# Optimization experiments

Measured on AMD Instinct MI355X. Metric: run time of the kernel, lower is better.

## Reference

```python
import jax, jax.numpy as jnp
import numpy as np

EPS = 1e-5
N_CAMERAS, N_POINTS = 6, 4


def _bilinear_sample(feats, gx, gy):
    # feats: [B, C, H, W]; gx, gy: [B, Q] in [-1, 1]; align_corners=False, zero padding
    B, C, H, W = feats.shape
    ix = ((gx + 1.0) * W - 1.0) * 0.5
    iy = ((gy + 1.0) * H - 1.0) * 0.5
    x0 = jnp.floor(ix)
    y0 = jnp.floor(iy)
    fx = ix - x0
    fy = iy - y0
    x0i = x0.astype(jnp.int32)
    y0i = y0.astype(jnp.int32)
    ff = feats.reshape(B, C, H * W)

    def corner(xi, yi, w):
        valid = (xi >= 0) & (xi < W) & (yi >= 0) & (yi < H)
        idx = jnp.clip(yi, 0, H - 1) * W + jnp.clip(xi, 0, W - 1)
        v = jnp.take_along_axis(ff, idx[:, None, :], axis=2)  # [B, C, Q]
        return v * (w * valid)[:, None, :]

    return (corner(x0i, y0i, (1 - fx) * (1 - fy))
            + corner(x0i + 1, y0i, fx * (1 - fy))
            + corner(x0i, y0i + 1, (1 - fx) * fy)
            + corner(x0i + 1, y0i + 1, fx * fy))


def setup_inputs() -> dict:
    key = jax.random.key(0)
    ks = jax.random.split(key, 8)
    Hb = Wb = 128
    nq = Hb * Wb
    bs, hidden, N, P = 2, 256, N_CAMERAS, N_POINTS
    C, Hf, Wf = 256, 28, 50

    rho = jnp.broadcast_to((jnp.arange(Hb, dtype=jnp.float32) / Hb)[:, None], (Hb, Wb))
    phi = jnp.broadcast_to((jnp.arange(Wb, dtype=jnp.float32) / Wb)[None, :], (Hb, Wb))
    pc_range = jnp.array([51.2, 2.0 * np.pi, -5.0, 3.0], jnp.float32)
    intervals = jnp.array([51.2 / Hb, 2.0 * np.pi / Wb], jnp.float32)
    img_size = jnp.array([1600.0, 900.0], jnp.float32)

    # realistic pinhole lidar->image matrices for 6 surround cameras
    K = np.array([[1200.0, 0, 800, 0], [0, 1200.0, 450, 0], [0, 0, 1, 0], [0, 0, 0, 1]], np.float32)
    mats = []
    for i in range(N):
        yaw = 2.0 * np.pi * i / N
        c, s = np.cos(yaw), np.sin(yaw)
        R = np.array([[s, -c, 0], [0, 0, -1], [c, s, 0]], np.float32)  # x_right, y_down, z_forward
        E = np.eye(4, dtype=np.float32)
        E[:3, :3] = R
        E[:3, 3] = np.array([0.0, 1.5, 0.5], np.float32)
        mats.append(K @ E)
    lidar2imgs = jnp.asarray(np.broadcast_to(np.stack(mats), (bs, N, 4, 4)).copy())

    return {
        'query': jax.random.normal(ks[0], (nq, bs, hidden), jnp.float32),
        'query_pos': jax.random.normal(ks[1], (nq, bs, hidden), jnp.float32),
        'rho': rho,
        'phi': phi,
        'zz_cord': jax.random.uniform(ks[2], (bs, nq, 1), jnp.float32),
        'img_feats': jax.random.normal(ks[3], (bs, N, C, Hf, Wf), jnp.float32),
        'lidar2imgs': lidar2imgs,
        'intervals': intervals,
        'pc_range': pc_range,
        'img_size': img_size,
        'Wa': jax.random.normal(ks[4], (hidden, N * P), jnp.float32) * 0.02,
        'ba': jnp.zeros((N * P,), jnp.float32),
        'Wo': jax.random.normal(ks[5], (hidden, hidden), jnp.float32) * 0.02,
        'bo': jnp.zeros((hidden,), jnp.float32),
    }


def reference(query, query_pos, rho, phi, zz_cord, img_feats, lidar2imgs,
              intervals, pc_range, img_size, Wa, ba, Wo, bo):
    q = jnp.transpose(query + query_pos, (1, 0, 2))  # [bs, nq, h]
    bs, nq, _ = q.shape
    aw = (q @ Wa + ba).reshape(bs, 1, nq, N_CAMERAS, N_POINTS)

    # polar BEV -> cartesian lidar coords
    r = rho.reshape(-1, 1) * pc_range[0] + intervals[0] / 2  # [nq, 1]
    p = phi.reshape(-1, 1) * pc_range[1] - jnp.pi + intervals[1] / 2
    xx = r * jnp.cos(p)
    yy = r * jnp.sin(p)
    zz = zz_cord * (pc_range[3] - pc_range[2]) + pc_range[2]  # [bs, nq, 1]
    xyz = jnp.concatenate([
        jnp.broadcast_to(xx[None], (bs, nq, 1)),
        jnp.broadcast_to(yy[None], (bs, nq, 1)),
        zz,
        jnp.ones((bs, nq, 1), q.dtype),
    ], axis=-1)  # [bs, nq, 4]

    cam = jnp.einsum('bnij,bqj->bnqi', lidar2imgs, xyz)  # [bs, N, nq, 4]
    zc = cam[..., 2]
    gx = cam[..., 0] / jnp.maximum(zc, EPS) / img_size[0]
    gy = cam[..., 1] / jnp.maximum(zc, EPS) / img_size[1]
    gx = (gx - 0.5) * 2.0
    gy = (gy - 0.5) * 2.0
    mask = (zc > EPS) & (gx > -1.0) & (gx < 1.0) & (gy > -1.0) & (gy < 1.0)  # [bs, N, nq]

    B, N, C, H, W = img_feats.shape
    sampled = _bilinear_sample(img_feats.reshape(B * N, C, H, W),
                               gx.reshape(B * N, nq), gy.reshape(B * N, nq))
    sampled = jnp.nan_to_num(sampled.reshape(B, N, C, nq).transpose(0, 2, 3, 1))  # [bs, C, nq, N]

    maskf = mask.transpose(0, 2, 1)[:, None, :, :, None].astype(q.dtype)  # [bs,1,nq,N,1]
    ws = (jax.nn.sigmoid(aw) * maskf).sum(-1)  # [bs, 1, nq, N]
    out = jnp.einsum('bcqn,bqn->bcq', sampled, ws[:, 0])  # [bs, C, nq]
    out = out.transpose(2, 0, 1) @ Wo + bo + query  # dropout p=0 -> identity
    mask_out = mask.transpose(0, 2, 1)[:, None, :, :, None]  # [bs,1,nq,N,1] bool
    return out, mask_out
```

## Files before the change

kernel.cpp:

```cpp
#include <hip/hip_runtime.h>
#include <math.h>

#define NQ    16384
#define BS    2
#define HID   256
#define NCAM  6
#define NPTS  4
#define CF    256
#define HF    28
#define WF    50
#define HWF   (HF*WF)
#define NIMG  (BS*NCAM)
#define EPSV  1e-5f
#define GQ    16

typedef __attribute__((ext_vector_type(8))) short short8v;
typedef __attribute__((ext_vector_type(4))) float float4v;

__device__ __forceinline__ unsigned short f2bf(float f) {
    unsigned u = __float_as_uint(f);
    u += 0x7fffu + ((u >> 16) & 1u);
    return (unsigned short)(u >> 16);
}
__device__ __forceinline__ float bfLO(unsigned u) { return __uint_as_float(u << 16); }
__device__ __forceinline__ float bfHI(unsigned u) { return __uint_as_float(u & 0xffff0000u); }

__global__ __launch_bounds__(256) void transpose_feats(
    const float* __restrict__ feats, unsigned short* __restrict__ featsT)
{
    __shared__ float tile[32][33];
    const int img = blockIdx.x / 44;
    const int hw0 = (blockIdx.x % 44) * 32;
    const int tx = threadIdx.x & 31;
    const int ty = threadIdx.x >> 5;
    for (int ct = 0; ct < 8; ++ct) {
        const int c0 = ct * 32;
        #pragma unroll
        for (int i = 0; i < 4; ++i) {
            const int c  = c0 + ty + 8 * i;
            const int hw = hw0 + tx;
            tile[ty + 8 * i][tx] = (hw < HWF) ? feats[((size_t)img * CF + c) * HWF + hw] : 0.f;
        }
        __syncthreads();
        #pragma unroll
        for (int i = 0; i < 4; ++i) {
            const int hw = hw0 + ty + 8 * i;
            if (hw < HWF)
                featsT[((size_t)img * HWF + hw) * CF + c0 + tx] = f2bf(tile[tx][ty + 8 * i]);
        }
        __syncthreads();
    }
}

__global__ __launch_bounds__(256) void transpose_wo_wa(
    const float* __restrict__ Wo, const float* __restrict__ Wa,
    unsigned short* __restrict__ WoT, unsigned short* __restrict__ WaT)
{
    if (blockIdx.x < 64) {
        __shared__ float tile[32][33];
        const int kt = blockIdx.x >> 3, nt = blockIdx.x & 7;
        const int tx = threadIdx.x & 31;
        const int ty = threadIdx.x >> 5;
        #pragma unroll
        for (int i = 0; i < 4; ++i)
            tile[ty + 8 * i][tx] = Wo[(size_t)(kt * 32 + ty + 8 * i) * HID + nt * 32 + tx];
        __syncthreads();
        #pragma unroll
        for (int i = 0; i < 4; ++i)
            WoT[(size_t)(nt * 32 + ty + 8 * i) * HID + kt * 32 + tx] = f2bf(tile[tx][ty + 8 * i]);
    } else {
        #pragma unroll
        for (int v = 0; v < 4; ++v) {
            const int idx = (blockIdx.x - 64) * 1024 + v * 256 + threadIdx.x;
            const int j = idx >> 8, k = idx & 255;
            WaT[idx] = (j < 24) ? f2bf(Wa[k * 24 + j]) : (unsigned short)0;
        }
    }
}

__global__ __launch_bounds__(512) void ca_fused3(
    const float* __restrict__ query, const float* __restrict__ query_pos,
    const float* __restrict__ rho,   const float* __restrict__ phi,
    const float* __restrict__ zz,    const unsigned short* __restrict__ featsT,
    const float* __restrict__ l2i,   const float* __restrict__ intervals,
    const float* __restrict__ pc_range, const float* __restrict__ img_size,
    const unsigned short* __restrict__ WaT, const float* __restrict__ ba,
    const unsigned short* __restrict__ WoT, const float* __restrict__ bo,
    float* __restrict__ out)
{
    __shared__ char  fab[GQ * 512];
    __shared__ float awl[GQ][36];

    const int tid  = threadIdx.x;
    const int wave = tid >> 6;
    const int lane = tid & 63;
    const int l32  = lane & 31;
    const int r    = wave * 2 + (lane >> 5);
    const int base = blockIdx.x * GQ;
    const int g    = base + r;
    const int b    = g >> 14;
    const int q    = g & (NQ - 1);
    const size_t qrow = ((size_t)q * BS + b) * HID;

    {
        const float4 a0 = *reinterpret_cast<const float4*>(&query[qrow + 8 * l32]);
        const float4 a1 = *reinterpret_cast<const float4*>(&query[qrow + 8 * l32 + 4]);
        const float4 p0 = *reinterpret_cast<const float4*>(&query_pos[qrow + 8 * l32]);
        const float4 p1 = *reinterpret_cast<const float4*>(&query_pos[qrow + 8 * l32 + 4]);
        uint4 u;
        u.x = ((unsigned)f2bf(a0.y + p0.y) << 16) | f2bf(a0.x + p0.x);
        u.y = ((unsigned)f2bf(a0.w + p0.w) << 16) | f2bf(a0.z + p0.z);
        u.z = ((unsigned)f2bf(a1.y + p1.y) << 16) | f2bf(a1.x + p1.x);
        u.w = ((unsigned)f2bf(a1.w + p1.w) << 16) | f2bf(a1.z + p1.z);
        *reinterpret_cast<uint4*>(fab + ((unsigned)(r * 512 + 16 * l32) ^ ((unsigned)(r & 7) << 4))) = u;
    }

    float gxs[NCAM], gys[NCAM];
    bool  msk[NCAM];
    {
        const float pc0 = pc_range[0], pc1 = pc_range[1];
        const float pc2 = pc_range[2], pc3 = pc_range[3];
        const float rr = rho[q] * pc0 + intervals[0] * 0.5f;
        const float pp = phi[q] * pc1 - 3.14159265358979323846f + intervals[1] * 0.5f;
        const float xx = rr * cosf(pp);
        const float yy = rr * sinf(pp);
        const float z  = zz[b * NQ + q] * (pc3 - pc2) + pc2;
        const float iw = img_size[0], ih = img_size[1];
        #pragma unroll
        for (int n = 0; n < NCAM; ++n) {
            const float* M = l2i + (b * NCAM + n) * 16;
            const float cx = M[0]*xx + M[1]*yy + M[2]*z  + M[3];
            const float cy = M[4]*xx + M[5]*yy + M[6]*z  + M[7];
            const float cz = M[8]*xx + M[9]*yy + M[10]*z + M[11];
            const float d  = fmaxf(cz, EPSV);
            const float gx = (cx / d / iw - 0.5f) * 2.0f;
            const float gy = (cy / d / ih - 0.5f) * 2.0f;
            msk[n] = (cz > EPSV) && (gx > -1.0f) && (gx < 1.0f)
                                 && (gy > -1.0f) && (gy < 1.0f);
            gxs[n] = gx; gys[n] = gy;
        }
    }
    if (l32 < NCAM)
        out[(size_t)NQ * BS * HID + ((size_t)b * NQ + q) * NCAM + l32] =
            msk[l32] ? 1.0f : 0.0f;

    __syncthreads();

    if (wave < 2) {
        const int arow = lane & 15;
        const int g4   = lane >> 4;
        float4v aw = {0.f, 0.f, 0.f, 0.f};
        #pragma unroll
        for (int kk = 0; kk < 8; ++kk) {
            const int k0 = kk * 32 + g4 * 8;
            const short8v af = *reinterpret_cast<const short8v*>(
                fab + ((unsigned)(arow * 512 + k0 * 2) ^ ((unsigned)(arow & 7) << 4)));
            const short8v bw = *reinterpret_cast<const short8v*>(
                WaT + (size_t)(wave * 16 + arow) * HID + k0);
            aw = __builtin_amdgcn_mfma_f32_16x16x32_bf16(af, bw, aw, 0, 0, 0);
        }
        #pragma unroll
        for (int i = 0; i < 4; ++i)
            awl[g4 * 4 + i][wave * 16 + arow] = aw[i];
    }
    __syncthreads();

    float wsv[NCAM];
    {
        float sv = 0.f;
        if (l32 < 24) {
            const float x = awl[r][l32] + ba[l32];
            sv = 1.0f / (1.0f + __expf(-x));
        }
        sv += __shfl_xor(sv, 1);
        sv += __shfl_xor(sv, 2);
        #pragma unroll
        for (int n = 0; n < NCAM; ++n)
            wsv[n] = __shfl(sv, (lane & 32) + 4 * n);
    }

    float acc[8] = {0.f, 0.f, 0.f, 0.f, 0.f, 0.f, 0.f, 0.f};
    for (int n = 0; n < NCAM; ++n) {
        if (msk[n]) {
            const float ixf = ((gxs[n] + 1.0f) * WF - 1.0f) * 0.5f;
            const float iyf = ((gys[n] + 1.0f) * HF - 1.0f) * 0.5f;
            const float x0f = floorf(ixf), y0f = floorf(iyf);
            const float fx = ixf - x0f, fy = iyf - y0f;
            const int x0 = (int)x0f, y0 = (int)y0f;
            const int   xs[4] = {x0, x0 + 1, x0,     x0 + 1};
            const int   ys[4] = {y0, y0,     y0 + 1, y0 + 1};
            const float wc[4] = {(1.f-fx)*(1.f-fy), fx*(1.f-fy),
                                 (1.f-fx)*fy,       fx*fy};
            const unsigned short* fb = featsT + (size_t)(b * NCAM + n) * HWF * CF + 8 * l32;
            #pragma unroll
            for (int c4 = 0; c4 < 4; ++c4) {
                const bool v = (xs[c4] >= 0) && (xs[c4] < WF) &&
                               (ys[c4] >= 0) && (ys[c4] < HF);
                const int xc = min(max(xs[c4], 0), WF - 1);
                const int yc = min(max(ys[c4], 0), HF - 1);
                const float wnv = wsv[n] * (v ? wc[c4] : 0.0f);
                const uint4 u = *reinterpret_cast<const uint4*>(fb + (size_t)(yc * WF + xc) * CF);
                acc[0] += wnv * bfLO(u.x); acc[1] += wnv * bfHI(u.x);
                acc[2] += wnv * bfLO(u.y); acc[3] += wnv * bfHI(u.y);
                acc[4] += wnv * bfLO(u.z); acc[5] += wnv * bfHI(u.z);
                acc[6] += wnv * bfLO(u.w); acc[7] += wnv * bfHI(u.w);
            }
        }
    }

    {
        uint4 u;
        u.x = ((unsigned)f2bf(acc[1]) << 16) | f2bf(acc[0]);
        u.y = ((unsigned)f2bf(acc[3]) << 16) | f2bf(acc[2]);
        u.z = ((unsigned)f2bf(acc[5]) << 16) | f2bf(acc[4]);
        u.w = ((unsigned)f2bf(acc[7]) << 16) | f2bf(acc[6]);
        *reinterpret_cast<uint4*>(fab + ((unsigned)(r * 512 + 16 * l32) ^ ((unsigned)(r & 7) << 4))) = u;
    }
    __syncthreads();

    const int colw = lane & 15;
    const int g4   = lane >> 4;
    #pragma unroll
    for (int t = 0; t < 2; ++t) {
        const int col = wave * 16 + t * 128 + colw;
        float4v dacc = {0.f, 0.f, 0.f, 0.f};
        #pragma unroll
        for (int kk = 0; kk < 8; ++kk) {
            const int k0 = kk * 32 + g4 * 8;
            const short8v af = *reinterpret_cast<const short8v*>(
                fab + ((unsigned)(colw * 512 + k0 * 2) ^ ((unsigned)(colw & 7) << 4)));
            const short8v bw = *reinterpret_cast<const short8v*>(
                WoT + (size_t)col * HID + k0);
            dacc = __builtin_amdgcn_mfma_f32_16x16x32_bf16(af, bw, dacc, 0, 0, 0);
        }
        #pragma unroll
        for (int rg = 0; rg < 4; ++rg) {
            const int rowq = g4 * 4 + rg;
            const int gq = base + rowq;
            const int bq = gq >> 14, qq = gq & (NQ - 1);
            const size_t addr = ((size_t)qq * BS + bq) * HID + col;
            out[addr] = dacc[rg] + bo[col] + query[addr];
        }
    }
}

#define CHUNK 32
__global__ __launch_bounds__(512, 2) void ca_fused_fb(
    const float* __restrict__ query, const float* __restrict__ query_pos,
    const float* __restrict__ rho, const float* __restrict__ phi,
    const float* __restrict__ zz, const float* __restrict__ feats,
    const float* __restrict__ l2i, const float* __restrict__ intervals,
    const float* __restrict__ pc_range, const float* __restrict__ img_size,
    const float* __restrict__ Wa, const float* __restrict__ ba,
    const float* __restrict__ Wo, const float* __restrict__ bo,
    float* __restrict__ out)
{
    __shared__ float fa[8][HID];
    __shared__ float wolds[CHUNK][HID];
    const int tid  = threadIdx.x;
    const int wave = tid >> 6;
    const int lane = tid & 63;
    const int g    = blockIdx.x * 8 + wave;
    const int b    = g / NQ;
    const int q    = g - b * NQ;
    const size_t qrow = ((size_t)q * BS + b) * HID;
    {
        float qv[4];
        #pragma unroll
        for (int k = 0; k < 4; ++k) {
            const int h = lane + 64 * k;
            qv[k] = query[qrow + h] + query_pos[qrow + h];
        }
        const float pc0 = pc_range[0], pc1 = pc_range[1];
        const float pc2 = pc_range[2], pc3 = pc_range[3];
        const float r = rho[q] * pc0 + intervals[0] * 0.5f;
        const float p = phi[q] * pc1 - 3.14159265358979323846f + intervals[1] * 0.5f;
        const float xx = r * cosf(p);
        const float yy = r * sinf(p);
        const float z  = zz[b * NQ + q] * (pc3 - pc2) + pc2;
        const float iw = img_size[0], ih = img_size[1];
        float gxs[NCAM], gys[NCAM], wss[NCAM];
        bool  msk[NCAM];
        #pragma unroll
        for (int n = 0; n < NCAM; ++n) {
            const float* M = l2i + (b * NCAM + n) * 16;
            const float cx = M[0]*xx + M[1]*yy + M[2]*z  + M[3];
            const float cy = M[4]*xx + M[5]*yy + M[6]*z  + M[7];
            const float cz = M[8]*xx + M[9]*yy + M[10]*z + M[11];
            const float d  = fmaxf(cz, EPSV);
            const float gx = (cx / d / iw - 0.5f) * 2.0f;
            const float gy = (cy / d / ih - 0.5f) * 2.0f;
            msk[n] = (cz > EPSV) && (gx > -1.0f) && (gx < 1.0f)
                                 && (gy > -1.0f) && (gy < 1.0f);
            gxs[n] = gx; gys[n] = gy; wss[n] = 0.0f;
        }
        for (int n = 0; n < NCAM; ++n) {
            if (!msk[n]) continue;
            float s = 0.0f;
            #pragma unroll
            for (int pp = 0; pp < NPTS; ++pp) {
                const int j = n * NPTS + pp;
                float part = 0.0f;
                #pragma unroll
                for (int k = 0; k < 4; ++k)
                    part += qv[k] * Wa[(lane + 64 * k) * 24 + j];
                #pragma unroll
                for (int off = 32; off; off >>= 1)
                    part += __shfl_xor(part, off, 64);
                s += 1.0f / (1.0f + expf(-(part + ba[j])));
            }
            wss[n] = s;
        }
        if (lane < NCAM)
            out[(size_t)NQ * BS * HID + ((size_t)b * NQ + q) * NCAM + lane] =
                msk[lane] ? 1.0f : 0.0f;
        float acc[4] = {0.f, 0.f, 0.f, 0.f};
        for (int n = 0; n < NCAM; ++n) {
            if (!msk[n]) continue;
            const float ixf = ((gxs[n] + 1.0f) * WF - 1.0f) * 0.5f;
            const float iyf = ((gys[n] + 1.0f) * HF - 1.0f) * 0.5f;
            const float x0f = floorf(ixf), y0f = floorf(iyf);
            const float fx = ixf - x0f, fy = iyf - y0f;
            const int x0 = (int)x0f, y0 = (int)y0f;
            const int   xs[4] = {x0, x0 + 1, x0,     x0 + 1};
            const int   ys[4] = {y0, y0,     y0 + 1, y0 + 1};
            const float wc[4] = {(1.f-fx)*(1.f-fy), fx*(1.f-fy),
                                 (1.f-fx)*fy,       fx*fy};
            int   offc[4];
            float wv[4];
            #pragma unroll
            for (int c4 = 0; c4 < 4; ++c4) {
                const bool v = (xs[c4] >= 0) && (xs[c4] < WF) &&
                               (ys[c4] >= 0) && (ys[c4] < HF);
                const int xc = min(max(xs[c4], 0), WF - 1);
                const int yc = min(max(ys[c4], 0), HF - 1);
                offc[c4] = yc * WF + xc;
                wv[c4]   = v ? wc[c4] : 0.0f;
            }
            const float wn = wss[n];
            const float* fbp = feats + (size_t)(b * NCAM + n) * CF * HWF;
            #pragma unroll
            for (int k = 0; k < 4; ++k) {
                const float* fc = fbp + (size_t)(lane + 64 * k) * HWF;
                const float sv = wv[0]*fc[offc[0]] + wv[1]*fc[offc[1]]
                               + wv[2]*fc[offc[2]] + wv[3]*fc[offc[3]];
                acc[k] += wn * sv;
            }
        }
        #pragma unroll
        for (int k = 0; k < 4; ++k)
            fa[wave][lane + 64 * k] = acc[k];
    }
    float racc[4] = {0.f, 0.f, 0.f, 0.f};
    const int h0 = 4 * lane;
    for (int c0 = 0; c0 < HID; c0 += CHUNK) {
        __syncthreads();
        for (int i = tid; i < CHUNK * HID; i += 512)
            wolds[i >> 8][i & 255] = Wo[(size_t)(c0 + (i >> 8)) * HID + (i & 255)];
        __syncthreads();
        #pragma unroll 8
        for (int c = 0; c < CHUNK; ++c) {
            const float fav = fa[wave][c0 + c];
            const float4 wv4 = *reinterpret_cast<const float4*>(&wolds[c][h0]);
            racc[0] += fav * wv4.x;
            racc[1] += fav * wv4.y;
            racc[2] += fav * wv4.z;
            racc[3] += fav * wv4.w;
        }
    }
    float4 o;
    o.x = racc[0] + bo[h0 + 0] + query[qrow + h0 + 0];
    o.y = racc[1] + bo[h0 + 1] + query[qrow + h0 + 1];
    o.z = racc[2] + bo[h0 + 2] + query[qrow + h0 + 2];
    o.w = racc[3] + bo[h0 + 3] + query[qrow + h0 + 3];
    *reinterpret_cast<float4*>(&out[qrow + h0]) = o;
}

extern "C" void kernel_launch(void* const* d_in, const int* in_sizes, int n_in,
                              void* d_out, int out_size, void* d_ws, size_t ws_size,
                              hipStream_t stream) {
    const float* query     = (const float*)d_in[0];
    const float* query_pos = (const float*)d_in[1];
    const float* rho       = (const float*)d_in[2];
    const float* phi       = (const float*)d_in[3];
    const float* zz        = (const float*)d_in[4];
    const float* feats     = (const float*)d_in[5];
    const float* l2i       = (const float*)d_in[6];
    const float* intervals = (const float*)d_in[7];
    const float* pc_range  = (const float*)d_in[8];
    const float* img_size  = (const float*)d_in[9];
    const float* Wa        = (const float*)d_in[10];
    const float* ba        = (const float*)d_in[11];
    const float* Wo        = (const float*)d_in[12];
    const float* bo        = (const float*)d_in[13];
    float* out = (float*)d_out;

    const size_t featsT_bytes = (size_t)NIMG * HWF * CF * 2;
    const size_t woT_bytes    = (size_t)HID * HID * 2;
    const size_t waT_bytes    = (size_t)32 * HID * 2;
    const size_t need = featsT_bytes + woT_bytes + waT_bytes;

    if (ws_size >= need) {
        unsigned short* featsT = (unsigned short*)d_ws;
        unsigned short* WoT    = (unsigned short*)((char*)d_ws + featsT_bytes);
        unsigned short* WaT    = (unsigned short*)((char*)d_ws + featsT_bytes + woT_bytes);
        transpose_feats<<<NIMG * 44, 256, 0, stream>>>(feats, featsT);
        transpose_wo_wa<<<72, 256, 0, stream>>>(Wo, Wa, WoT, WaT);
        ca_fused3<<<(BS * NQ) / GQ, 512, 0, stream>>>(query, query_pos, rho, phi, zz,
                                                      featsT, l2i, intervals, pc_range,
                                                      img_size, WaT, ba, WoT, bo, out);
    } else {
        ca_fused_fb<<<(BS * NQ) / 8, 512, 0, stream>>>(query, query_pos, rho, phi, zz,
                                                       feats, l2i, intervals, pc_range,
                                                       img_size, Wa, ba, Wo, bo, out);
    }
}
```

Baseline: 79.48 us.

## Split fused kernel into attention-weight, gather and tiled GEMM kernels

```diff
diff --git a/kernel.cpp b/kernel.cpp
--- a/kernel.cpp
+++ b/kernel.cpp
@@ -12,7 +12,6 @@
 #define HWF   (HF*WF)
 #define NIMG  (BS*NCAM)
 #define EPSV  1e-5f
-#define GQ    16
 
 typedef __attribute__((ext_vector_type(8))) short short8v;
 typedef __attribute__((ext_vector_type(4))) float float4v;
@@ -25,42 +24,37 @@
 __device__ __forceinline__ float bfLO(unsigned u) { return __uint_as_float(u << 16); }
 __device__ __forceinline__ float bfHI(unsigned u) { return __uint_as_float(u & 0xffff0000u); }
 
-__global__ __launch_bounds__(256) void transpose_feats(
-    const float* __restrict__ feats, unsigned short* __restrict__ featsT)
+__global__ __launch_bounds__(256) void prep_all(
+    const float* __restrict__ feats, const float* __restrict__ Wo,
+    const float* __restrict__ Wa, unsigned short* __restrict__ featsT,
+    unsigned short* __restrict__ WoT, unsigned short* __restrict__ WaT)
 {
     __shared__ float tile[32][33];
-    const int img = blockIdx.x / 44;
-    const int hw0 = (blockIdx.x % 44) * 32;
     const int tx = threadIdx.x & 31;
     const int ty = threadIdx.x >> 5;
-    for (int ct = 0; ct < 8; ++ct) {
-        const int c0 = ct * 32;
-        #pragma unroll
-        for (int i = 0; i < 4; ++i) {
-            const int c  = c0 + ty + 8 * i;
-            const int hw = hw0 + tx;
-            tile[ty + 8 * i][tx] = (hw < HWF) ? feats[((size_t)img * CF + c) * HWF + hw] : 0.f;
-        }
-        __syncthreads();
-        #pragma unroll
-        for (int i = 0; i < 4; ++i) {
-            const int hw = hw0 + ty + 8 * i;
-            if (hw < HWF)
-                featsT[((size_t)img * HWF + hw) * CF + c0 + tx] = f2bf(tile[tx][ty + 8 * i]);
-        }
-        __syncthreads();
-    }
-}
-
-__global__ __launch_bounds__(256) void transpose_wo_wa(
-    const float* __restrict__ Wo, const float* __restrict__ Wa,
-    unsigned short* __restrict__ WoT, unsigned short* __restrict__ WaT)
-{
-    if (blockIdx.x < 64) {
-        __shared__ float tile[32][33];
-        const int kt = blockIdx.x >> 3, nt = blockIdx.x & 7;
-        const int tx = threadIdx.x & 31;
-        const int ty = threadIdx.x >> 5;
+    if (blockIdx.x < 528) {
+        const int img = blockIdx.x / 44;
+        const int hw0 = (blockIdx.x % 44) * 32;
+        for (int ct = 0; ct < 8; ++ct) {
+            const int c0 = ct * 32;
+            #pragma unroll
+            for (int i = 0; i < 4; ++i) {
+                const int c  = c0 + ty + 8 * i;
+                const int hw = hw0 + tx;
+                tile[ty + 8 * i][tx] = (hw < HWF) ? feats[((size_t)img * CF + c) * HWF + hw] : 0.f;
+            }
+            __syncthreads();
+            #pragma unroll
+            for (int i = 0; i < 4; ++i) {
+                const int hw = hw0 + ty + 8 * i;
+                if (hw < HWF)
+                    featsT[((size_t)img * HWF + hw) * CF + c0 + tx] = f2bf(tile[tx][ty + 8 * i]);
+            }
+            __syncthreads();
+        }
+    } else if (blockIdx.x < 592) {
+        const int bid = blockIdx.x - 528;
+        const int kt = bid >> 3, nt = bid & 7;
         #pragma unroll
         for (int i = 0; i < 4; ++i)
             tile[ty + 8 * i][tx] = Wo[(size_t)(kt * 32 + ty + 8 * i) * HID + nt * 32 + tx];
@@ -69,54 +63,85 @@
         for (int i = 0; i < 4; ++i)
             WoT[(size_t)(nt * 32 + ty + 8 * i) * HID + kt * 32 + tx] = f2bf(tile[tx][ty + 8 * i]);
     } else {
+        const int bid = blockIdx.x - 592;
         #pragma unroll
         for (int v = 0; v < 4; ++v) {
-            const int idx = (blockIdx.x - 64) * 1024 + v * 256 + threadIdx.x;
+            const int idx = bid * 1024 + v * 256 + threadIdx.x;
             const int j = idx >> 8, k = idx & 255;
             WaT[idx] = (j < 24) ? f2bf(Wa[k * 24 + j]) : (unsigned short)0;
         }
     }
 }
 
-__global__ __launch_bounds__(512) void ca_fused3(
+__global__ __launch_bounds__(256) void k_aw(
     const float* __restrict__ query, const float* __restrict__ query_pos,
-    const float* __restrict__ rho,   const float* __restrict__ phi,
-    const float* __restrict__ zz,    const unsigned short* __restrict__ featsT,
-    const float* __restrict__ l2i,   const float* __restrict__ intervals,
+    const unsigned short* __restrict__ WaT, const float* __restrict__ ba,
+    float* __restrict__ ws)
+{
+    const int wave = threadIdx.x >> 6;
+    const int lane = threadIdx.x & 63;
+    const int arow = lane & 15;
+    const int g4   = lane >> 4;
+    const int g0   = (blockIdx.x * 4 + wave) * 16;
+    const int ga   = g0 + arow;
+    const int bb   = ga >> 14;
+    const int qq   = ga & (NQ - 1);
+    const float* qp1 = query     + ((size_t)qq * BS + bb) * HID;
+    const float* qp2 = query_pos + ((size_t)qq * BS + bb) * HID;
+
+    float4v aw0 = {0.f,0.f,0.f,0.f}, aw1 = {0.f,0.f,0.f,0.f};
+    #pragma unroll
+    for (int kk = 0; kk < 8; ++kk) {
+        const int k0 = kk * 32 + g4 * 8;
+        const float4 a0 = *reinterpret_cast<const float4*>(qp1 + k0);
+        const float4 a1 = *reinterpret_cast<const float4*>(qp1 + k0 + 4);
+        const float4 p0 = *reinterpret_cast<const float4*>(qp2 + k0);
+        const float4 p1 = *reinterpret_cast<const float4*>(qp2 + k0 + 4);
+        short8v af;
+        af[0] = (short)f2bf(a0.x + p0.x); af[1] = (short)f2bf(a0.y + p0.y);
+        af[2] = (short)f2bf(a0.z + p0.z); af[3] = (short)f2bf(a0.w + p0.w);
+        af[4] = (short)f2bf(a1.x + p1.x); af[5] = (short)f2bf(a1.y + p1.y);
+        af[6] = (short)f2bf(a1.z + p1.z); af[7] = (short)f2bf(a1.w + p1.w);
+        const short8v b0 = *reinterpret_cast<const short8v*>(WaT + (size_t)arow * HID + k0);
+        const short8v b1 = *reinterpret_cast<const short8v*>(WaT + (size_t)(16 + arow) * HID + k0);
+        aw0 = __builtin_amdgcn_mfma_f32_16x16x32_bf16(af, b0, aw0, 0, 0, 0);
+        aw1 = __builtin_amdgcn_mfma_f32_16x16x32_bf16(af, b1, aw1, 0, 0, 0);
+    }
+    const float ba0 = ba[arow];
+    const float ba1 = (arow < 8) ? ba[16 + arow] : 0.f;
+    #pragma unroll
+    for (int i = 0; i < 4; ++i) {
+        float s0 = 1.0f / (1.0f + __expf(-(aw0[i] + ba0)));
+        float s1 = (arow < 8) ? 1.0f / (1.0f + __expf(-(aw1[i] + ba1))) : 0.f;
+        s0 += __shfl_xor(s0, 1);  s0 += __shfl_xor(s0, 2);
+        s1 += __shfl_xor(s1, 1);  s1 += __shfl_xor(s1, 2);
+        if ((arow & 3) == 0) {
+            const int gq = g0 + g4 * 4 + i;
+            ws[(size_t)gq * 8 + (arow >> 2)] = s0;
+            if (arow < 8)
+                ws[(size_t)gq * 8 + 4 + (arow >> 2)] = s1;
+        }
+    }
+}
+
+__global__ __launch_bounds__(512) void k_gather(
+    const float* __restrict__ rho, const float* __restrict__ phi,
+    const float* __restrict__ zz, const unsigned short* __restrict__ featsT,
+    const float* __restrict__ l2i, const float* __restrict__ intervals,
     const float* __restrict__ pc_range, const float* __restrict__ img_size,
-    const unsigned short* __restrict__ WaT, const float* __restrict__ ba,
-    const unsigned short* __restrict__ WoT, const float* __restrict__ bo,
+    const float* __restrict__ ws, unsigned short* __restrict__ fa,
     float* __restrict__ out)
 {
-    __shared__ char  fab[GQ * 512];
-    __shared__ float awl[GQ][36];
-
-    const int tid  = threadIdx.x;
-    const int wave = tid >> 6;
-    const int lane = tid & 63;
+    const int lane = threadIdx.x & 63;
+    const int wave = threadIdx.x >> 6;
     const int l32  = lane & 31;
     const int r    = wave * 2 + (lane >> 5);
-    const int base = blockIdx.x * GQ;
-    const int g    = base + r;
+    const int g    = blockIdx.x * 16 + r;
     const int b    = g >> 14;
     const int q    = g & (NQ - 1);
-    const size_t qrow = ((size_t)q * BS + b) * HID;
-
-    {
-        const float4 a0 = *reinterpret_cast<const float4*>(&query[qrow + 8 * l32]);
-        const float4 a1 = *reinterpret_cast<const float4*>(&query[qrow + 8 * l32 + 4]);
-        const float4 p0 = *reinterpret_cast<const float4*>(&query_pos[qrow + 8 * l32]);
-        const float4 p1 = *reinterpret_cast<const float4*>(&query_pos[qrow + 8 * l32 + 4]);
-        uint4 u;
-        u.x = ((unsigned)f2bf(a0.y + p0.y) << 16) | f2bf(a0.x + p0.x);
-        u.y = ((unsigned)f2bf(a0.w + p0.w) << 16) | f2bf(a0.z + p0.z);
-        u.z = ((unsigned)f2bf(a1.y + p1.y) << 16) | f2bf(a1.x + p1.x);
-        u.w = ((unsigned)f2bf(a1.w + p1.w) << 16) | f2bf(a1.z + p1.z);
-        *reinterpret_cast<uint4*>(fab + ((unsigned)(r * 512 + 16 * l32) ^ ((unsigned)(r & 7) << 4))) = u;
-    }
-
+
+    bool  msk[NCAM];
     float gxs[NCAM], gys[NCAM];
-    bool  msk[NCAM];
     {
         const float pc0 = pc_range[0], pc1 = pc_range[1];
         const float pc2 = pc_range[2], pc3 = pc_range[3];
@@ -140,16 +165,196 @@
             gxs[n] = gx; gys[n] = gy;
         }
     }
+    {
+        unsigned mbits = 0;
+        #pragma unroll
+        for (int n = 0; n < NCAM; ++n) mbits |= (msk[n] ? 1u : 0u) << n;
+        if (l32 < NCAM)
+            out[(size_t)NQ * BS * HID + ((size_t)b * NQ + q) * NCAM + l32] =
+                ((mbits >> l32) & 1u) ? 1.0f : 0.0f;
+    }
+
+    float wsv[NCAM];
+    {
+        const float wsn = ws[(size_t)g * 8 + (l32 & 7)];
+        #pragma unroll
+        for (int n = 0; n < NCAM; ++n)
+            wsv[n] = msk[n] ? __shfl(wsn, (lane & 32) + n) : 0.f;
+    }
+
+    float acc[8] = {0.f,0.f,0.f,0.f,0.f,0.f,0.f,0.f};
+    for (int n = 0; n < NCAM; ++n) {
+        if (!msk[n]) continue;
+        const float ixf = ((gxs[n] + 1.0f) * WF - 1.0f) * 0.5f;
+        const float iyf = ((gys[n] + 1.0f) * HF - 1.0f) * 0.5f;
+        const float x0f = floorf(ixf), y0f = floorf(iyf);
+        const float fx = ixf - x0f, fy = iyf - y0f;
+        const int x0 = (int)x0f, y0 = (int)y0f;
+        const int   xs[4] = {x0, x0 + 1, x0,     x0 + 1};
+        const int   ys[4] = {y0, y0,     y0 + 1, y0 + 1};
+        const float wc[4] = {(1.f-fx)*(1.f-fy), fx*(1.f-fy),
+                             (1.f-fx)*fy,       fx*fy};
+        const unsigned short* fb = featsT + (size_t)(b * NCAM + n) * HWF * CF + 8 * l32;
+        #pragma unroll
+        for (int c4 = 0; c4 < 4; ++c4) {
+            const bool v = (xs[c4] >= 0) && (xs[c4] < WF) &&
+                           (ys[c4] >= 0) && (ys[c4] < HF);
+            const int xc = min(max(xs[c4], 0), WF - 1);
+            const int yc = min(max(ys[c4], 0), HF - 1);
+            const float w = wsv[n] * (v ? wc[c4] : 0.0f);
+            const uint4 u = *reinterpret_cast<const uint4*>(fb + (size_t)(yc * WF + xc) * CF);
+            acc[0] += w * bfLO(u.x); acc[1] += w * bfHI(u.x);
+            acc[2] += w * bfLO(u.y); acc[3] += w * bfHI(u.y);
+            acc[4] += w * bfLO(u.z); acc[5] += w * bfHI(u.z);
+            acc[6] += w * bfLO(u.w); acc[7] += w * bfHI(u.w);
+        }
+    }
+
+    uint4 u;
+    u.x = ((unsigned)f2bf(acc[1]) << 16) | f2bf(acc[0]);
+    u.y = ((unsigned)f2bf(acc[3]) << 16) | f2bf(acc[2]);
+    u.z = ((unsigned)f2bf(acc[5]) << 16) | f2bf(acc[4]);
+    u.w = ((unsigned)f2bf(acc[7]) << 16) | f2bf(acc[6]);
+    *reinterpret_cast<uint4*>(fa + (size_t)g * HID + 8 * l32) = u;
+}
+
+__global__ __launch_bounds__(512) void k_gemm(
+    const unsigned short* __restrict__ fa, const unsigned short* __restrict__ WoT,
+    const float* __restrict__ bo, const float* __restrict__ query,
+    float* __restrict__ out)
+{
+    const int wave = threadIdx.x >> 6;
+    const int lane = threadIdx.x & 63;
+    const int arow = lane & 15;
+    const int g4   = lane >> 4;
+    const int wm   = wave >> 2;
+    const int wn   = wave & 3;
+    const int m0   = blockIdx.x * 128;
+
+    const unsigned short* aptr = fa  + (size_t)(m0 + wm * 64 + arow) * HID;
+    const unsigned short* bptr = WoT + (size_t)(wn * 64 + arow) * HID;
+
+    float4v acc00={0.f,0.f,0.f,0.f}, acc01={0.f,0.f,0.f,0.f}, acc02={0.f,0.f,0.f,0.f}, acc03={0.f,0.f,0.f,0.f};
+    float4v acc10={0.f,0.f,0.f,0.f}, acc11={0.f,0.f,0.f,0.f}, acc12={0.f,0.f,0.f,0.f}, acc13={0.f,0.f,0.f,0.f};
+    float4v acc20={0.f,0.f,0.f,0.f}, acc21={0.f,0.f,0.f,0.f}, acc22={0.f,0.f,0.f,0.f}, acc23={0.f,0.f,0.f,0.f};
+    float4v acc30={0.f,0.f,0.f,0.f}, acc31={0.f,0.f,0.f,0.f}, acc32={0.f,0.f,0.f,0.f}, acc33={0.f,0.f,0.f,0.f};
+
+    #pragma unroll 2
+    for (int kk = 0; kk < 8; ++kk) {
+        const int k0 = kk * 32 + g4 * 8;
+        short8v af0 = *reinterpret_cast<const short8v*>(aptr + 0 * 16 * HID + k0);
+        short8v af1 = *reinterpret_cast<const short8v*>(aptr + 1 * 16 * HID + k0);
+        short8v af2 = *reinterpret_cast<const short8v*>(aptr + 2 * 16 * HID + k0);
+        short8v af3 = *reinterpret_cast<const short8v*>(aptr + 3 * 16 * HID + k0);
+        short8v bf0 = *reinterpret_cast<const short8v*>(bptr + 0 * 16 * HID + k0);
+        short8v bf1 = *reinterpret_cast<const short8v*>(bptr + 1 * 16 * HID + k0);
+        short8v bf2 = *reinterpret_cast<const short8v*>(bptr + 2 * 16 * HID + k0);
+        short8v bf3 = *reinterpret_cast<const short8v*>(bptr + 3 * 16 * HID + k0);
+        acc00 = __builtin_amdgcn_mfma_f32_16x16x32_bf16(af0, bf0, acc00, 0, 0, 0);
+        acc01 = __builtin_amdgcn_mfma_f32_16x16x32_bf16(af0, bf1, acc01, 0, 0, 0);
+        acc02 = __builtin_amdgcn_mfma_f32_16x16x32_bf16(af0, bf2, acc02, 0, 0, 0);
+        acc03 = __builtin_amdgcn_mfma_f32_16x16x32_bf16(af0, bf3, acc03, 0, 0, 0);
+        acc10 = __builtin_amdgcn_mfma_f32_16x16x32_bf16(af1, bf0, acc10, 0, 0, 0);
+        acc11 = __builtin_amdgcn_mfma_f32_16x16x32_bf16(af1, bf1, acc11, 0, 0, 0);
+        acc12 = __builtin_amdgcn_mfma_f32_16x16x32_bf16(af1, bf2, acc12, 0, 0, 0);
+        acc13 = __builtin_amdgcn_mfma_f32_16x16x32_bf16(af1, bf3, acc13, 0, 0, 0);
+        acc20 = __builtin_amdgcn_mfma_f32_16x16x32_bf16(af2, bf0, acc20, 0, 0, 0);
+        acc21 = __builtin_amdgcn_mfma_f32_16x16x32_bf16(af2, bf1, acc21, 0, 0, 0);
+        acc22 = __builtin_amdgcn_mfma_f32_16x16x32_bf16(af2, bf2, acc22, 0, 0, 0);
+        acc23 = __builtin_amdgcn_mfma_f32_16x16x32_bf16(af2, bf3, acc23, 0, 0, 0);
+        acc30 = __builtin_amdgcn_mfma_f32_16x16x32_bf16(af3, bf0, acc30, 0, 0, 0);
+        acc31 = __builtin_amdgcn_mfma_f32_16x16x32_bf16(af3, bf1, acc31, 0, 0, 0);
+        acc32 = __builtin_amdgcn_mfma_f32_16x16x32_bf16(af3, bf2, acc32, 0, 0, 0);
+        acc33 = __builtin_amdgcn_mfma_f32_16x16x32_bf16(af3, bf3, acc33, 0, 0, 0);
+    }
+
+    float4v* accs[4][4] = {{&acc00,&acc01,&acc02,&acc03},{&acc10,&acc11,&acc12,&acc13},
+                           {&acc20,&acc21,&acc22,&acc23},{&acc30,&acc31,&acc32,&acc33}};
+    #pragma unroll
+    for (int j = 0; j < 4; ++j) {
+        const int col = wn * 64 + j * 16 + arow;
+        const float boc = bo[col];
+        #pragma unroll
+        for (int i = 0; i < 4; ++i) {
+            const float4v av = *accs[i][j];
+            #pragma unroll
+            for (int rg = 0; rg < 4; ++rg) {
+                const int m  = m0 + wm * 64 + i * 16 + g4 * 4 + rg;
+                const int bq = m >> 14, qq = m & (NQ - 1);
+                const size_t addr = ((size_t)qq * BS + bq) * HID + col;
+                out[addr] = av[rg] + boc + query[addr];
+            }
+        }
+    }
+}
+
+__global__ __launch_bounds__(512) void ca_fused3(
+    const float* __restrict__ query, const float* __restrict__ query_pos,
+    const float* __restrict__ rho,   const float* __restrict__ phi,
+    const float* __restrict__ zz,    const unsigned short* __restrict__ featsT,
+    const float* __restrict__ l2i,   const float* __restrict__ intervals,
+    const float* __restrict__ pc_range, const float* __restrict__ img_size,
+    const unsigned short* __restrict__ WaT, const float* __restrict__ ba,
+    const unsigned short* __restrict__ WoT, const float* __restrict__ bo,
+    float* __restrict__ out)
+{
+    __shared__ char  fab[16 * 512];
+    __shared__ float awl[16][36];
+    const int tid  = threadIdx.x;
+    const int wave = tid >> 6;
+    const int lane = tid & 63;
+    const int l32  = lane & 31;
+    const int r    = wave * 2 + (lane >> 5);
+    const int base = blockIdx.x * 16;
+    const int g    = base + r;
+    const int b    = g >> 14;
+    const int q    = g & (NQ - 1);
+    const size_t qrow = ((size_t)q * BS + b) * HID;
+    {
+        const float4 a0 = *reinterpret_cast<const float4*>(&query[qrow + 8 * l32]);
+        const float4 a1 = *reinterpret_cast<const float4*>(&query[qrow + 8 * l32 + 4]);
+        const float4 p0 = *reinterpret_cast<const float4*>(&query_pos[qrow + 8 * l32]);
+        const float4 p1 = *reinterpret_cast<const float4*>(&query_pos[qrow + 8 * l32 + 4]);
+        uint4 u;
+        u.x = ((unsigned)f2bf(a0.y + p0.y) << 16) | f2bf(a0.x + p0.x);
+        u.y = ((unsigned)f2bf(a0.w + p0.w) << 16) | f2bf(a0.z + p0.z);
+        u.z = ((unsigned)f2bf(a1.y + p1.y) << 16) | f2bf(a1.x + p1.x);
+        u.w = ((unsigned)f2bf(a1.w + p1.w) << 16) | f2bf(a1.z + p1.z);
+        *reinterpret_cast<uint4*>(fab + ((unsigned)(r * 512 + 16 * l32) ^ ((unsigned)(r & 7) << 4))) = u;
+    }
+    float gxs[NCAM], gys[NCAM];
+    bool  msk[NCAM];
+    {
+        const float pc0 = pc_range[0], pc1 = pc_range[1];
+        const float pc2 = pc_range[2], pc3 = pc_range[3];
+        const float rr = rho[q] * pc0 + intervals[0] * 0.5f;
+        const float pp = phi[q] * pc1 - 3.14159265358979323846f + intervals[1] * 0.5f;
+        const float xx = rr * cosf(pp);
+        const float yy = rr * sinf(pp);
+        const float z  = zz[b * NQ + q] * (pc3 - pc2) + pc2;
+        const float iw = img_size[0], ih = img_size[1];
+        #pragma unroll
+        for (int n = 0; n < NCAM; ++n) {
+            const float* M = l2i + (b * NCAM + n) * 16;
+            const float cx = M[0]*xx + M[1]*yy + M[2]*z  + M[3];
+            const float cy = M[4]*xx + M[5]*yy + M[6]*z  + M[7];
+            const float cz = M[8]*xx + M[9]*yy + M[10]*z + M[11];
+            const float d  = fmaxf(cz, EPSV);
+            const float gx = (cx / d / iw - 0.5f) * 2.0f;
+            const float gy = (cy / d / ih - 0.5f) * 2.0f;
+            msk[n] = (cz > EPSV) && (gx > -1.0f) && (gx < 1.0f)
+                                 && (gy > -1.0f) && (gy < 1.0f);
+            gxs[n] = gx; gys[n] = gy;
+        }
+    }
     if (l32 < NCAM)
         out[(size_t)NQ * BS * HID + ((size_t)b * NQ + q) * NCAM + l32] =
             msk[l32] ? 1.0f : 0.0f;
-
     __syncthreads();
-
     if (wave < 2) {
         const int arow = lane & 15;
         const int g4   = lane >> 4;
-        float4v aw = {0.f, 0.f, 0.f, 0.f};
+        float4v aw = {0.f,0.f,0.f,0.f};
         #pragma unroll
         for (int kk = 0; kk < 8; ++kk) {
             const int k0 = kk * 32 + g4 * 8;
@@ -164,7 +369,6 @@
             awl[g4 * 4 + i][wave * 16 + arow] = aw[i];
     }
     __syncthreads();
-
     float wsv[NCAM];
     {
         float sv = 0.f;
@@ -178,8 +382,7 @@
         for (int n = 0; n < NCAM; ++n)
             wsv[n] = __shfl(sv, (lane & 32) + 4 * n);
     }
-
-    float acc[8] = {0.f, 0.f, 0.f, 0.f, 0.f, 0.f, 0.f, 0.f};
+    float acc[8] = {0.f,0.f,0.f,0.f,0.f,0.f,0.f,0.f};
     for (int n = 0; n < NCAM; ++n) {
         if (msk[n]) {
             const float ixf = ((gxs[n] + 1.0f) * WF - 1.0f) * 0.5f;
@@ -207,7 +410,6 @@
             }
         }
     }
-
     {
         uint4 u;
         u.x = ((unsigned)f2bf(acc[1]) << 16) | f2bf(acc[0]);
@@ -217,13 +419,12 @@
         *reinterpret_cast<uint4*>(fab + ((unsigned)(r * 512 + 16 * l32) ^ ((unsigned)(r & 7) << 4))) = u;
     }
     __syncthreads();
-
     const int colw = lane & 15;
     const int g4   = lane >> 4;
     #pragma unroll
     for (int t = 0; t < 2; ++t) {
         const int col = wave * 16 + t * 128 + colw;
-        float4v dacc = {0.f, 0.f, 0.f, 0.f};
+        float4v dacc = {0.f,0.f,0.f,0.f};
         #pragma unroll
         for (int kk = 0; kk < 8; ++kk) {
             const int k0 = kk * 32 + g4 * 8;
@@ -235,8 +436,8 @@
         }
         #pragma unroll
         for (int rg = 0; rg < 4; ++rg) {
-            const int rowq = g4 * 4 + rg;
-            const int gq = base + rowq;
+            const int row = g4 * 4 + rg;
+            const int gq = base + row;
             const int bq = gq >> 14, qq = gq & (NQ - 1);
             const size_t addr = ((size_t)qq * BS + bq) * HID + col;
             out[addr] = dacc[rg] + bo[col] + query[addr];
@@ -314,7 +515,7 @@
         if (lane < NCAM)
             out[(size_t)NQ * BS * HID + ((size_t)b * NQ + q) * NCAM + lane] =
                 msk[lane] ? 1.0f : 0.0f;
-        float acc[4] = {0.f, 0.f, 0.f, 0.f};
+        float acc[4] = {0.f,0.f,0.f,0.f};
         for (int n = 0; n < NCAM; ++n) {
             if (!msk[n]) continue;
             const float ixf = ((gxs[n] + 1.0f) * WF - 1.0f) * 0.5f;
@@ -351,7 +552,7 @@
         for (int k = 0; k < 4; ++k)
             fa[wave][lane + 64 * k] = acc[k];
     }
-    float racc[4] = {0.f, 0.f, 0.f, 0.f};
+    float racc[4] = {0.f,0.f,0.f,0.f};
     const int h0 = 4 * lane;
     for (int c0 = 0; c0 < HID; c0 += CHUNK) {
         __syncthreads();
@@ -398,17 +599,30 @@
     const size_t featsT_bytes = (size_t)NIMG * HWF * CF * 2;
     const size_t woT_bytes    = (size_t)HID * HID * 2;
     const size_t waT_bytes    = (size_t)32 * HID * 2;
-    const size_t need = featsT_bytes + woT_bytes + waT_bytes;
-
-    if (ws_size >= need) {
+    const size_t ws_bytes     = (size_t)BS * NQ * 8 * 4;
+    const size_t fa_bytes     = (size_t)BS * NQ * HID * 2;
+    const size_t need_small   = featsT_bytes + woT_bytes + waT_bytes;
+    const size_t need_full    = need_small + ws_bytes + fa_bytes;
+
+    if (ws_size >= need_full) {
         unsigned short* featsT = (unsigned short*)d_ws;
         unsigned short* WoT    = (unsigned short*)((char*)d_ws + featsT_bytes);
         unsigned short* WaT    = (unsigned short*)((char*)d_ws + featsT_bytes + woT_bytes);
-        transpose_feats<<<NIMG * 44, 256, 0, stream>>>(feats, featsT);
-        transpose_wo_wa<<<72, 256, 0, stream>>>(Wo, Wa, WoT, WaT);
-        ca_fused3<<<(BS * NQ) / GQ, 512, 0, stream>>>(query, query_pos, rho, phi, zz,
-                                                      featsT, l2i, intervals, pc_range,
-                                                      img_size, WaT, ba, WoT, bo, out);
+        float*          wsb    = (float*)((char*)d_ws + need_small);
+        unsigned short* fab    = (unsigned short*)((char*)d_ws + need_small + ws_bytes);
+        prep_all<<<600, 256, 0, stream>>>(feats, Wo, Wa, featsT, WoT, WaT);
+        k_aw<<<512, 256, 0, stream>>>(query, query_pos, WaT, ba, wsb);
+        k_gather<<<2048, 512, 0, stream>>>(rho, phi, zz, featsT, l2i, intervals,
+                                           pc_range, img_size, wsb, fab, out);
+        k_gemm<<<256, 512, 0, stream>>>(fab, WoT, bo, query, out);
+    } else if (ws_size >= need_small) {
+        unsigned short* featsT = (unsigned short*)d_ws;
+        unsigned short* WoT    = (unsigned short*)((char*)d_ws + featsT_bytes);
+        unsigned short* WaT    = (unsigned short*)((char*)d_ws + featsT_bytes + woT_bytes);
+        prep_all<<<600, 256, 0, stream>>>(feats, Wo, Wa, featsT, WoT, WaT);
+        ca_fused3<<<2048, 512, 0, stream>>>(query, query_pos, rho, phi, zz,
+                                            featsT, l2i, intervals, pc_range,
+                                            img_size, WaT, ba, WoT, bo, out);
     } else {
         ca_fused_fb<<<(BS * NQ) / 8, 512, 0, stream>>>(query, query_pos, rho, phi, zz,
                                                        feats, l2i, intervals, pc_range,
```

Result: slower. 85.53 us (+7.6%).
